# Kernel tuning notes

Hardware: AMD Instinct MI355X
Metric: run time of the kernel (lower is better)

The kernel has to match this reference:

```python
import jax, jax.numpy as jnp
import numpy as np

B, S, D = 1, 4096, 1024
H = 16
HD = D // H  # 64
ROPE_THETA = 10000.0
NEG_INF = -1e9


def setup_inputs() -> dict:
    key = jax.random.key(0)
    ks = jax.random.split(key, 6)
    x = jax.random.normal(ks[0], (B, S, D), dtype=jnp.float32)
    # rotary frequencies: freqs_cis = exp(i * t * theta^{-2j/hd}), j in [0, hd/2)
    inv_freq = 1.0 / (ROPE_THETA ** (jnp.arange(0, HD, 2, dtype=jnp.float32) / HD))  # [HD/2]
    angles = jnp.arange(S, dtype=jnp.float32)[:, None] * inv_freq[None, :]  # [S, HD/2]
    freqs_cos = jnp.cos(angles)
    freqs_sin = jnp.sin(angles)
    # causal additive mask [S, S]
    mask = jnp.where(jnp.triu(jnp.ones((S, S), dtype=bool), k=1), NEG_INF, 0.0).astype(jnp.float32)
    scale = 0.02
    wq = jax.random.normal(ks[1], (D, D), dtype=jnp.float32) * scale
    wk = jax.random.normal(ks[2], (D, D), dtype=jnp.float32) * scale
    wv = jax.random.normal(ks[3], (D, D), dtype=jnp.float32) * scale
    wo = jax.random.normal(ks[4], (D, D), dtype=jnp.float32) * scale
    return {"x": x, "freqs_cos": freqs_cos, "freqs_sin": freqs_sin, "mask": mask,
            "wq": wq, "wk": wk, "wv": wv, "wo": wo}


def _apply_rope(t, cos, sin):
    # t: [B, S, H, HD]; cos/sin: [S, HD/2] -> broadcast [1, S, 1, HD/2]
    tr = t.reshape(*t.shape[:-1], HD // 2, 2)
    te, to = tr[..., 0], tr[..., 1]
    c = cos[None, :, None, :]
    s = sin[None, :, None, :]
    # complex multiply (te + i*to) * (c + i*s)
    oe = te * c - to * s
    oo = te * s + to * c
    return jnp.stack([oe, oo], axis=-1).reshape(t.shape)


def reference(x, freqs_cos, freqs_sin, mask, wq, wk, wv, wo):
    b, s, d = x.shape
    q = (x @ wq.T).reshape(b, s, H, HD)
    k = (x @ wk.T).reshape(b, s, H, HD)
    v = (x @ wv.T).reshape(b, s, H, HD)
    q = _apply_rope(q, freqs_cos, freqs_sin)
    k = _apply_rope(k, freqs_cos, freqs_sin)
    # [B, H, S, HD]
    q = q.transpose(0, 2, 1, 3)
    k = k.transpose(0, 2, 1, 3)
    v = v.transpose(0, 2, 1, 3)
    scores = jnp.einsum('bhqd,bhkd->bhqk', q, k) / jnp.sqrt(jnp.float32(HD))
    scores = scores + mask[None, None, :, :]
    probs = jax.nn.softmax(scores.astype(jnp.float32), axis=-1).astype(q.dtype)
    out = jnp.einsum('bhqk,bhkd->bhqd', probs, v)
    out = out.transpose(0, 2, 1, 3).reshape(b, s, d)
    return out @ wo.T
```

## Files before the change

### kernel.cpp

```cpp
#include <hip/hip_runtime.h>
#include <stdint.h>

typedef _Float16 f16;
typedef _Float16 v2h __attribute__((ext_vector_type(2)));
typedef _Float16 v4h __attribute__((ext_vector_type(4)));
typedef _Float16 v8h __attribute__((ext_vector_type(8)));
typedef float    v4f __attribute__((ext_vector_type(4)));
typedef __fp16   v2fp __attribute__((ext_vector_type(2)));

#define SEQ 4096
#define NH  16
#define DM  1024
#define QSCALE 0.18033688011112042f
#define MBASE 8.0f

__device__ __forceinline__ float exp2_(float x) {
#if __has_builtin(__builtin_amdgcn_exp2f)
  return __builtin_amdgcn_exp2f(x);
#else
  return exp2f(x);
#endif
}

__device__ __forceinline__ v2h pkrtz(float a, float b) {
  v2fp r = __builtin_amdgcn_cvt_pkrtz(a, b);
  return __builtin_bit_cast(v2h, r);
}

__device__ __forceinline__ void gload_lds16(const void* g, void* l) {
  __builtin_amdgcn_global_load_lds((const __attribute__((address_space(1))) void*)g,
                                   (__attribute__((address_space(3))) void*)l,
                                   16, 0, 0);
}

#define NX 4194304
#define NW 1048576
__global__ void convert_kernel(const float* __restrict__ x,
                               const float* __restrict__ wq, const float* __restrict__ wk,
                               const float* __restrict__ wv, const float* __restrict__ wo,
                               f16* __restrict__ xf, f16* __restrict__ W, f16* __restrict__ Wo) {
  size_t e = ((size_t)blockIdx.x * 256 + threadIdx.x) * 4;
  const float* src; f16* dst;
  if (e < (size_t)NX) { src = x + e; dst = xf + e; }
  else {
    size_t j = e - NX; int wi = (int)(j >> 20); size_t off = j & (NW - 1);
    src = (wi == 0 ? wq : wi == 1 ? wk : wi == 2 ? wv : wo) + off;
    dst = (wi < 3 ? W + (size_t)wi * NW : Wo) + off;
  }
  v4f v = *(const v4f*)src;
  v4h o = { (f16)v.x, (f16)v.y, (f16)v.z, (f16)v.w };
  *(v4h*)dst = o;
}

__global__ __launch_bounds__(256, 3) void gemm_qkv_kernel(const f16* __restrict__ A,
                                                          const f16* __restrict__ B,
                                                          const float* __restrict__ fc,
                                                          const float* __restrict__ fs,
                                                          f16* __restrict__ Qh,
                                                          f16* __restrict__ Kh,
                                                          f16* __restrict__ Vt) {
  const int K = 1024;
  __shared__ __align__(16) f16 SM[16640];
  f16* As = SM;
  f16* Bs = SM + 8192;
  const int t = threadIdx.x;
  const int w = t >> 6, l = t & 63, quad = l >> 4, l15 = l & 15;
  const int wm = w & 1, wn = w >> 1;
  const int bx = blockIdx.x;
  const int m0 = blockIdx.y * 128, n0 = bx * 128;

  v4f acc[4][4];
#pragma unroll
  for (int i = 0; i < 4; ++i)
#pragma unroll
    for (int j = 0; j < 4; ++j) acc[i][j] = v4f{0.f, 0.f, 0.f, 0.f};

  for (int kt = 0; kt < 16; ++kt) {
    __syncthreads();
#pragma unroll
    for (int i = 0; i < 4; ++i) {
      int c = i * 256 + t; int r = c >> 3, cc = c & 7; int sc = cc ^ (r & 7);
      gload_lds16(A + (size_t)(m0 + r) * K + kt * 64 + sc * 8, As + c * 8);
      gload_lds16(B + (size_t)(n0 + r) * K + kt * 64 + sc * 8, Bs + c * 8);
    }
    __syncthreads();
#pragma unroll
    for (int ks = 0; ks < 2; ++ks) {
      v8h af[4], bf[4];
#pragma unroll
      for (int i = 0; i < 4; ++i) {
        int ra = wm * 64 + i * 16 + l15;
        af[i] = *(const v8h*)(As + ra * 64 + (((ks * 4 + quad) ^ (ra & 7)) * 8));
        int rb = wn * 64 + i * 16 + l15;
        bf[i] = *(const v8h*)(Bs + rb * 64 + (((ks * 4 + quad) ^ (rb & 7)) * 8));
      }
#pragma unroll
      for (int i = 0; i < 4; ++i)
#pragma unroll
        for (int j = 0; j < 4; ++j)
          acc[i][j] = __builtin_amdgcn_mfma_f32_16x16x32_f16(af[i], bf[j], acc[i][j], 0, 0, 0);
    }
  }
  const int mat = bx >> 3;
  if (mat < 2) {
    __syncthreads();
    float* FC = (float*)SM;
    float* FS = FC + 4096;
    {
      const v4f* s4c = (const v4f*)(fc + (size_t)m0 * 32);
      const v4f* s4s = (const v4f*)(fs + (size_t)m0 * 32);
      v4f* d4c = (v4f*)FC;
      v4f* d4s = (v4f*)FS;
#pragma unroll
      for (int k = 0; k < 4; ++k) {
        int idx = k * 256 + t;
        d4c[idx] = s4c[idx];
        d4s[idx] = s4s[idx];
      }
    }
    __syncthreads();
    f16* dst = (mat == 0) ? Qh : Kh;
    const int hh = (bx & 7) * 2 + wn;
    const int mrow = wm * 64 + quad * 4;
#pragma unroll
    for (int j = 0; j < 4; ++j) {
      const int d = j * 16 + l15;
      const int i2 = d >> 1;
      const float sgnmul = (l15 & 1) ? 1.f : -1.f;
#pragma unroll
      for (int i = 0; i < 4; ++i) {
#pragma unroll
        for (int rg = 0; rg < 4; ++rg) {
          float own = acc[i][j][rg];
          float par = __shfl_xor(own, 1);
          int ml = mrow + i * 16 + rg;
          float c = FC[ml * 32 + i2], sn = FS[ml * 32 + i2];
          if (mat == 0) { c *= QSCALE; sn *= QSCALE; }
          float out = own * c + par * (sn * sgnmul);
          dst[((size_t)(hh * 4096 + m0 + ml)) * 64 + d] = (f16)out;
        }
      }
    }
  } else {
    __syncthreads();
    f16* T = SM;
#pragma unroll
    for (int i = 0; i < 4; ++i) {
      int srow = wm * 64 + i * 16 + quad * 4;
#pragma unroll
      for (int j = 0; j < 4; ++j) {
        int dd = wn * 64 + j * 16 + l15;
#pragma unroll
        for (int rg = 0; rg < 4; ++rg)
          T[(srow + rg) * 130 + dd] = (f16)acc[i][j][rg];
      }
    }
    __syncthreads();
    const int hv0 = (bx - 16) * 2;
#pragma unroll
    for (int loop = 0; loop < 16; ++loop) {
      int flat = loop * 256 + t;
      int dd = flat >> 5;
      int rem = flat & 31;
      int g = rem >> 3, kapc = rem & 7;
      int q = kapc >> 1, b = kapc & 1;
      int sb = g * 32 + 16 * b + 4 * q;
      v4h v = { T[(sb + 0) * 130 + dd], T[(sb + 1) * 130 + dd],
                T[(sb + 2) * 130 + dd], T[(sb + 3) * 130 + dd] };
      int h = hv0 + (dd >> 6), d = dd & 63;
      *(v4h*)(Vt + (size_t)(h * 64 + d) * 4096 + m0 + g * 32 + kapc * 4) = v;
    }
  }
}

__global__ __launch_bounds__(256, 4) void flash_kernel(const f16* __restrict__ Qh,
                                                       const f16* __restrict__ Kh,
                                                       const f16* __restrict__ Vt,
                                                       f16* __restrict__ Opart,
                                                       float* __restrict__ Lpart) {
  __shared__ __align__(16) f16 SM[16384];
  f16* Ks = SM;
  f16* Vs = SM + 8192;
  const int h = blockIdx.x & 15;
  const int sr = 79 - ((int)blockIdx.x >> 4);
  int qb, sp, nsp;
  if (sr < 8)       { qb = sr; sp = 0; nsp = 1; }
  else if (sr < 24) { int j = sr - 8;  qb = 8  + (j >> 1); sp = j & 1; nsp = 2; }
  else if (sr < 48) { int j = sr - 24; int q3 = j / 3; qb = 16 + q3; sp = j - 3 * q3; nsp = 3; }
  else              { int j = sr - 48; qb = 24 + (j >> 2); sp = j & 3; nsp = 4; }
  const int S = 2 * qb + 2;
  const int lo = (sp * S) / nsp, hi = ((sp + 1) * S) / nsp - 1;

  const int t = threadIdx.x, w = t >> 6, l = t & 63, quad = l >> 4, l15 = l & 15;
  const int q0w = qb * 128 + w * 32;

  v8h qf[2][2];
#pragma unroll
  for (int qt = 0; qt < 2; ++qt)
#pragma unroll
    for (int ks = 0; ks < 2; ++ks)
      qf[qt][ks] = *(const v8h*)(Qh + ((size_t)(h * 4096 + q0w + qt * 16 + l15)) * 64 + ks * 32 + quad * 8);

  v8h onesh;
#pragma unroll
  for (int j = 0; j < 8; ++j) onesh[j] = (f16)1.f;

  v4f av[2][4];
  v4f avl[2];
#pragma unroll
  for (int qt = 0; qt < 2; ++qt) {
    avl[qt] = v4f{0.f, 0.f, 0.f, 0.f};
#pragma unroll
    for (int db = 0; db < 4; ++db) av[qt][db] = v4f{0.f, 0.f, 0.f, 0.f};
  }

  const int c0 = t, c1 = 256 + t;
  const int r0 = c0 >> 3, sc0 = (c0 & 7) ^ (r0 & 7);
  const int r1 = c1 >> 3, sc1 = (c1 & 7) ^ (r1 & 7);
  const f16* KhB = Kh + (size_t)h * 4096 * 64;
  const f16* VtB = Vt + (size_t)h * 64 * 4096;

  {
    int koff = lo * 64;
    f16* Kd = Ks + (lo & 1) * 4096;
    f16* Vd = Vs + (lo & 1) * 4096;
    gload_lds16(KhB + (size_t)(koff + r0) * 64 + sc0 * 8, Kd + c0 * 8);
    gload_lds16(KhB + (size_t)(koff + r1) * 64 + sc1 * 8, Kd + c1 * 8);
    gload_lds16(VtB + (size_t)r0 * 4096 + koff + sc0 * 8, Vd + c0 * 8);
    gload_lds16(VtB + (size_t)r1 * 4096 + koff + sc1 * 8, Vd + c1 * 8);
  }

  for (int kb = lo; kb <= hi; ++kb) {
    __syncthreads();
    if (kb < hi) {
      int nb = (kb + 1) & 1;
      int koff = (kb + 1) * 64;
      gload_lds16(KhB + (size_t)(koff + r0) * 64 + sc0 * 8, Ks + nb * 4096 + c0 * 8);
      gload_lds16(KhB + (size_t)(koff + r1) * 64 + sc1 * 8, Ks + nb * 4096 + c1 * 8);
      gload_lds16(VtB + (size_t)r0 * 4096 + koff + sc0 * 8, Vs + nb * 4096 + c0 * 8);
      gload_lds16(VtB + (size_t)r1 * 4096 + koff + sc1 * 8, Vs + nb * 4096 + c1 * 8);
    }
    if (kb * 64 > q0w + 31) continue;
    const f16* Kc = Ks + (kb & 1) * 4096;
    const f16* Vc = Vs + (kb & 1) * 4096;

    v8h kf[4][2];
#pragma unroll
    for (int kt = 0; kt < 4; ++kt)
#pragma unroll
      for (int ks = 0; ks < 2; ++ks) {
        int r = kt * 16 + l15;
        kf[kt][ks] = *(const v8h*)(Kc + r * 64 + (((ks * 4 + quad) ^ (r & 7)) * 8));
      }

    union { v8h v8[2]; v2h v2[8]; } P[2];
#pragma unroll
    for (int qt = 0; qt < 2; ++qt) {
      int qtb = q0w + qt * 16;
      v4f st[4];
#pragma unroll
      for (int kt = 0; kt < 4; ++kt) {
        v4f z = v4f{ -MBASE, -MBASE, -MBASE, -MBASE };
        z = __builtin_amdgcn_mfma_f32_16x16x32_f16(kf[kt][0], qf[qt][0], z, 0, 0, 0);
        st[kt] = __builtin_amdgcn_mfma_f32_16x16x32_f16(kf[kt][1], qf[qt][1], z, 0, 0, 0);
      }
      if (kb * 64 + 63 > qtb) {
        int qg = qtb + l15;
#pragma unroll
        for (int kt = 0; kt < 4; ++kt)
#pragma unroll
          for (int jj = 0; jj < 4; ++jj) {
            int kg = kb * 64 + kt * 16 + quad * 4 + jj;
            if (kg > qg) st[kt][jj] = -1e30f;
          }
      }
#pragma unroll
      for (int kt = 0; kt < 4; ++kt) {
        float p0 = exp2_(st[kt][0]), p1 = exp2_(st[kt][1]);
        float p2 = exp2_(st[kt][2]), p3 = exp2_(st[kt][3]);
        P[qt].v2[kt * 2 + 0] = pkrtz(p0, p1);
        P[qt].v2[kt * 2 + 1] = pkrtz(p2, p3);
      }
#pragma unroll
      for (int g = 0; g < 2; ++g)
        avl[qt] = __builtin_amdgcn_mfma_f32_16x16x32_f16(onesh, P[qt].v8[g], avl[qt], 0, 0, 0);
    }

#pragma unroll
    for (int db = 0; db < 4; ++db) {
      int r = db * 16 + l15;
#pragma unroll
      for (int g = 0; g < 2; ++g) {
        v8h vf = *(const v8h*)(Vc + r * 64 + (((g * 4 + quad) ^ (r & 7)) * 8));
        av[0][db] = __builtin_amdgcn_mfma_f32_16x16x32_f16(vf, P[0].v8[g], av[0][db], 0, 0, 0);
        av[1][db] = __builtin_amdgcn_mfma_f32_16x16x32_f16(vf, P[1].v8[g], av[1][db], 0, 0, 0);
      }
    }
  }
  const size_t base = (size_t)(h * 80 + sr);
#pragma unroll
  for (int qt = 0; qt < 2; ++qt) {
    int q = w * 32 + qt * 16 + l15;
    if (quad == 0) Lpart[base * 128 + q] = avl[qt][0];
#pragma unroll
    for (int db = 0; db < 4; ++db) {
      v4h o = { (f16)av[qt][db][0], (f16)av[qt][db][1],
                (f16)av[qt][db][2], (f16)av[qt][db][3] };
      *(v4h*)(Opart + base * 8192 + (size_t)q * 64 + db * 16 + quad * 4) = o;
    }
  }
}

__global__ void combine_kernel(const f16* __restrict__ Opart, const float* __restrict__ Lpart,
                               f16* __restrict__ attn) {
  int qb = blockIdx.x, h = blockIdx.y;
  int nsp, base;
  if (qb < 8)       { nsp = 1; base = qb; }
  else if (qb < 16) { nsp = 2; base = 8 + 2 * (qb - 8); }
  else if (qb < 24) { nsp = 3; base = 24 + 3 * (qb - 16); }
  else              { nsp = 4; base = 48 + 4 * (qb - 24); }
  int t = threadIdx.x, q = t >> 1, dh = (t & 1) * 32;
  float l = 0.f;
  float o[32];
#pragma unroll
  for (int c = 0; c < 32; ++c) o[c] = 0.f;
  for (int s = 0; s < nsp; ++s) {
    size_t sb = (size_t)(h * 80 + base + s);
    const f16* P = Opart + sb * 8192 + q * 64 + dh;
#pragma unroll
    for (int c = 0; c < 4; ++c) {
      v8h v = *(const v8h*)(P + c * 8);
#pragma unroll
      for (int j = 0; j < 8; ++j) o[c * 8 + j] += (float)v[j];
    }
    l += Lpart[sb * 128 + q];
  }
  float inv = 1.f / l;
#pragma unroll
  for (int c = 0; c < 4; ++c) {
    v8h v;
#pragma unroll
    for (int j = 0; j < 8; ++j) v[j] = (f16)(o[c * 8 + j] * inv);
    *(v8h*)(attn + (size_t)(qb * 128 + q) * 1024 + h * 64 + dh + c * 8) = v;
  }
}

__global__ __launch_bounds__(256, 3) void gemm_out_kernel(const f16* __restrict__ A,
                                                          const f16* __restrict__ B,
                                                          float* __restrict__ C) {
  const int K = 1024, N = 1024;
  __shared__ __align__(16) f16 As[128 * 64];
  __shared__ __align__(16) f16 Bs[64 * 64];
  const int t = threadIdx.x;
  const int w = t >> 6, l = t & 63, quad = l >> 4, l15 = l & 15;
  const int wm = w & 1, wn = w >> 1;
  const int m0 = blockIdx.y * 128, n0 = blockIdx.x * 64;

  v4f acc[4][2];
#pragma unroll
  for (int i = 0; i < 4; ++i)
#pragma unroll
    for (int j = 0; j < 2; ++j) acc[i][j] = v4f{0.f, 0.f, 0.f, 0.f};

  for (int kt = 0; kt < 16; ++kt) {
    __syncthreads();
#pragma unroll
    for (int i = 0; i < 4; ++i) {
      int c = i * 256 + t; int r = c >> 3, cc = c & 7; int sc = cc ^ (r & 7);
      gload_lds16(A + (size_t)(m0 + r) * K + kt * 64 + sc * 8, As + c * 8);
    }
#pragma unroll
    for (int i = 0; i < 2; ++i) {
      int c = i * 256 + t; int r = c >> 3, cc = c & 7; int sc = cc ^ (r & 7);
      gload_lds16(B + (size_t)(n0 + r) * K + kt * 64 + sc * 8, Bs + c * 8);
    }
    __syncthreads();
#pragma unroll
    for (int ks = 0; ks < 2; ++ks) {
      v8h af[4], bf[2];
#pragma unroll
      for (int i = 0; i < 4; ++i) {
        int ra = wm * 64 + i * 16 + l15;
        af[i] = *(const v8h*)(As + ra * 64 + (((ks * 4 + quad) ^ (ra & 7)) * 8));
      }
#pragma unroll
      for (int j = 0; j < 2; ++j) {
        int rb = wn * 32 + j * 16 + l15;
        bf[j] = *(const v8h*)(Bs + rb * 64 + (((ks * 4 + quad) ^ (rb & 7)) * 8));
      }
#pragma unroll
      for (int i = 0; i < 4; ++i)
#pragma unroll
        for (int j = 0; j < 2; ++j)
          acc[i][j] = __builtin_amdgcn_mfma_f32_16x16x32_f16(af[i], bf[j], acc[i][j], 0, 0, 0);
    }
  }
#pragma unroll
  for (int i = 0; i < 4; ++i) {
    int m = m0 + wm * 64 + i * 16 + quad * 4;
#pragma unroll
    for (int j = 0; j < 2; ++j) {
      int n = n0 + wn * 32 + j * 16 + l15;
#pragma unroll
      for (int rg = 0; rg < 4; ++rg)
        C[(size_t)(m + rg) * N + n] = acc[i][j][rg];
    }
  }
}

extern "C" void kernel_launch(void* const* d_in, const int* in_sizes, int n_in,
                              void* d_out, int out_size, void* d_ws, size_t ws_size,
                              hipStream_t stream) {
  (void)in_sizes; (void)n_in; (void)out_size; (void)ws_size;
  const float* x  = (const float*)d_in[0];
  const float* fc = (const float*)d_in[1];
  const float* fs = (const float*)d_in[2];
  const float* wq = (const float*)d_in[4];
  const float* wk = (const float*)d_in[5];
  const float* wv = (const float*)d_in[6];
  const float* wo = (const float*)d_in[7];
  float* out = (float*)d_out;
  char* ws = (char*)d_ws;

  f16* xf    = (f16*)(ws);
  f16* W     = (f16*)(ws + 8388608);
  f16* Wo    = (f16*)(ws + 14680064);
  f16* Opart = (f16*)(ws + 16777216);
  float* Lpart = (float*)(ws + 16777216 + 20971520);
  f16* Qh    = (f16*)(ws + 41943040);
  f16* Kh    = (f16*)(ws + 50331648);
  f16* Vt    = (f16*)(ws + 58720256);
  f16* attn  = xf;

  convert_kernel<<<dim3(8192), dim3(256), 0, stream>>>(x, wq, wk, wv, wo, xf, W, Wo);
  gemm_qkv_kernel<<<dim3(24, 32), dim3(256), 0, stream>>>(xf, W, fc, fs, Qh, Kh, Vt);
  flash_kernel<<<dim3(1280), dim3(256), 0, stream>>>(Qh, Kh, Vt, Opart, Lpart);
  combine_kernel<<<dim3(32, 16), dim3(256), 0, stream>>>(Opart, Lpart, attn);
  gemm_out_kernel<<<dim3(16, 32), dim3(256), 0, stream>>>(attn, Wo, out);
}
```

Before: 277.6 us.

## Remap GEMM blocks per XCD for L2 reuse and skip masked q-tiles in flash

Both GEMM kernels now use a 1D grid with a block index remap, so blocks on the same XCD (round-robin by b&7) share the same N column tiles of the weight matrix. This is meant to improve L2 locality on the multi-XCD chip. In the flash kernel, the per-warp loop over the two 16-row query tiles now skips a tile whose rows are entirely above the current key block. The P·V MFMAs move inside that per-tile loop, so fully masked tiles skip both the exp work and the PV work. The trade-off is that V fragments are reloaded from LDS once per query tile instead of being shared by both.

```diff
diff --git a/kernel.cpp b/kernel.cpp
--- a/kernel.cpp
+++ b/kernel.cpp
@@ -66,8 +66,10 @@
   const int t = threadIdx.x;
   const int w = t >> 6, l = t & 63, quad = l >> 4, l15 = l & 15;
   const int wm = w & 1, wn = w >> 1;
-  const int bx = blockIdx.x;
-  const int m0 = blockIdx.y * 128, n0 = bx * 128;
+  const int b = blockIdx.x, xcd = b & 7, g = b >> 3;
+  const int bx = xcd * 3 + (g % 3);
+  const int m0 = (g / 3) * 128;
+  const int n0 = bx * 128;
 
   v4f acc[4][4];
 #pragma unroll
@@ -162,13 +164,13 @@
       int flat = loop * 256 + t;
       int dd = flat >> 5;
       int rem = flat & 31;
-      int g = rem >> 3, kapc = rem & 7;
-      int q = kapc >> 1, b = kapc & 1;
-      int sb = g * 32 + 16 * b + 4 * q;
+      int gg = rem >> 3, kapc = rem & 7;
+      int q = kapc >> 1, bb = kapc & 1;
+      int sb = gg * 32 + 16 * bb + 4 * q;
       v4h v = { T[(sb + 0) * 130 + dd], T[(sb + 1) * 130 + dd],
                 T[(sb + 2) * 130 + dd], T[(sb + 3) * 130 + dd] };
       int h = hv0 + (dd >> 6), d = dd & 63;
-      *(v4h*)(Vt + (size_t)(h * 64 + d) * 4096 + m0 + g * 32 + kapc * 4) = v;
+      *(v4h*)(Vt + (size_t)(h * 64 + d) * 4096 + m0 + gg * 32 + kapc * 4) = v;
     }
   }
 }
@@ -253,10 +255,10 @@
         kf[kt][ks] = *(const v8h*)(Kc + r * 64 + (((ks * 4 + quad) ^ (r & 7)) * 8));
       }
 
-    union { v8h v8[2]; v2h v2[8]; } P[2];
 #pragma unroll
     for (int qt = 0; qt < 2; ++qt) {
       int qtb = q0w + qt * 16;
+      if (kb * 64 > qtb + 15) continue;
       v4f st[4];
 #pragma unroll
       for (int kt = 0; kt < 4; ++kt) {
@@ -274,26 +276,25 @@
             if (kg > qg) st[kt][jj] = -1e30f;
           }
       }
+      union { v8h v8[2]; v2h v2[8]; } P;
 #pragma unroll
       for (int kt = 0; kt < 4; ++kt) {
         float p0 = exp2_(st[kt][0]), p1 = exp2_(st[kt][1]);
         float p2 = exp2_(st[kt][2]), p3 = exp2_(st[kt][3]);
-        P[qt].v2[kt * 2 + 0] = pkrtz(p0, p1);
-        P[qt].v2[kt * 2 + 1] = pkrtz(p2, p3);
+        P.v2[kt * 2 + 0] = pkrtz(p0, p1);
+        P.v2[kt * 2 + 1] = pkrtz(p2, p3);
       }
 #pragma unroll
       for (int g = 0; g < 2; ++g)
-        avl[qt] = __builtin_amdgcn_mfma_f32_16x16x32_f16(onesh, P[qt].v8[g], avl[qt], 0, 0, 0);
-    }
-
-#pragma unroll
-    for (int db = 0; db < 4; ++db) {
-      int r = db * 16 + l15;
-#pragma unroll
-      for (int g = 0; g < 2; ++g) {
-        v8h vf = *(const v8h*)(Vc + r * 64 + (((g * 4 + quad) ^ (r & 7)) * 8));
-        av[0][db] = __builtin_amdgcn_mfma_f32_16x16x32_f16(vf, P[0].v8[g], av[0][db], 0, 0, 0);
-        av[1][db] = __builtin_amdgcn_mfma_f32_16x16x32_f16(vf, P[1].v8[g], av[1][db], 0, 0, 0);
+        avl[qt] = __builtin_amdgcn_mfma_f32_16x16x32_f16(onesh, P.v8[g], avl[qt], 0, 0, 0);
+#pragma unroll
+      for (int db = 0; db < 4; ++db) {
+        int r = db * 16 + l15;
+#pragma unroll
+        for (int g = 0; g < 2; ++g) {
+          v8h vf = *(const v8h*)(Vc + r * 64 + (((g * 4 + quad) ^ (r & 7)) * 8));
+          av[qt][db] = __builtin_amdgcn_mfma_f32_16x16x32_f16(vf, P.v8[g], av[qt][db], 0, 0, 0);
+        }
       }
     }
   }
@@ -354,7 +355,9 @@
   const int t = threadIdx.x;
   const int w = t >> 6, l = t & 63, quad = l >> 4, l15 = l & 15;
   const int wm = w & 1, wn = w >> 1;
-  const int m0 = blockIdx.y * 128, n0 = blockIdx.x * 64;
+  const int b = blockIdx.x, xcd = b & 7, g = b >> 3;
+  const int n0 = (xcd * 2 + (g & 1)) * 64;
+  const int m0 = (g >> 1) * 128;
 
   v4f acc[4][2];
 #pragma unroll
@@ -433,8 +436,8 @@
   f16* attn  = xf;
 
   convert_kernel<<<dim3(8192), dim3(256), 0, stream>>>(x, wq, wk, wv, wo, xf, W, Wo);
-  gemm_qkv_kernel<<<dim3(24, 32), dim3(256), 0, stream>>>(xf, W, fc, fs, Qh, Kh, Vt);
+  gemm_qkv_kernel<<<dim3(768), dim3(256), 0, stream>>>(xf, W, fc, fs, Qh, Kh, Vt);
   flash_kernel<<<dim3(1280), dim3(256), 0, stream>>>(Qh, Kh, Vt, Opart, Lpart);
   combine_kernel<<<dim3(32, 16), dim3(256), 0, stream>>>(Opart, Lpart, attn);
-  gemm_out_kernel<<<dim3(16, 32), dim3(256), 0, stream>>>(attn, Wo, out);
-}
+  gemm_out_kernel<<<dim3(512), dim3(256), 0, stream>>>(attn, Wo, out);
+}
```

Result: faster. 240.7 us (-13.3%).
